# Kernel optimization log

Hardware: AMD Instinct MI355X
Metric: run time of the kernel (lower is better)

Reference implementation:

```python
import jax, jax.numpy as jnp
from jax import lax
import numpy as np

H = 32  # hidden_size


def setup_inputs() -> dict:
    key = jax.random.key(0)
    ks = jax.random.split(key, 12)
    B, T, I = 4096, 1024, 1
    s = lambda fan_in: 1.0 / np.sqrt(fan_in)
    inp = {
        "x": jax.random.normal(ks[0], (B, I, T), dtype=jnp.float32),
        # LSTM params, PyTorch layout: gates stacked as [i, f, g, o]
        "W_ih": jax.random.uniform(ks[1], (4 * H, I), jnp.float32, -s(H), s(H)),
        "W_hh": jax.random.uniform(ks[2], (4 * H, H), jnp.float32, -s(H), s(H)),
        "b_ih": jax.random.uniform(ks[3], (4 * H,), jnp.float32, -s(H), s(H)),
        "b_hh": jax.random.uniform(ks[4], (4 * H,), jnp.float32, -s(H), s(H)),
        # MLP head: 32 -> 16 -> 8 -> 1
        "W1": jax.random.uniform(ks[5], (16, H), jnp.float32, -s(H), s(H)),
        "b1": jax.random.uniform(ks[6], (16,), jnp.float32, -s(H), s(H)),
        "W2": jax.random.uniform(ks[7], (8, 16), jnp.float32, -s(16), s(16)),
        "b2": jax.random.uniform(ks[8], (8,), jnp.float32, -s(16), s(16)),
        "W3": jax.random.uniform(ks[9], (1, 8), jnp.float32, -s(8), s(8)),
        "b3": jax.random.uniform(ks[10], (1,), jnp.float32, -s(8), s(8)),
    }
    return inp


def reference(x, W_ih, W_hh, b_ih, b_hh, W1, b1, W2, b2, W3, b3):
    # x: (B, 1, T) -> (B, T, 1), batch_first LSTM over T
    xs = jnp.transpose(x, (0, 2, 1))
    B, T, _ = xs.shape
    # Precompute input contribution to all gates: (B, T, 4H)
    xW = jnp.einsum('bti,gi->btg', xs, W_ih) + (b_ih + b_hh)

    def step(carry, xw_t):
        h, c = carry
        gates = xw_t + h @ W_hh.T  # (B, 4H)
        i, f, g, o = jnp.split(gates, 4, axis=-1)
        c = jax.nn.sigmoid(f) * c + jax.nn.sigmoid(i) * jnp.tanh(g)
        h = jax.nn.sigmoid(o) * jnp.tanh(c)
        return (h, c), None

    h0 = jnp.zeros((B, H), xs.dtype)
    (h_n, _), _ = lax.scan(step, (h0, h0), jnp.swapaxes(xW, 0, 1))

    # MLP head on final hidden state h_n[-1] (single layer -> h_n itself)
    out = jax.nn.relu(h_n @ W1.T + b1)
    out = jax.nn.relu(out @ W2.T + b2)
    return out @ W3.T + b3  # (B, 1)
```

## Files before the change

### kernel.cpp

```cpp
#include <hip/hip_runtime.h>

#define HSZ 32
#define TT  1024

__device__ __forceinline__ float frcp(float x) { return __builtin_amdgcn_rcpf(x); }
__device__ __forceinline__ float sigm(float z) { return frcp(1.0f + __expf(-z)); }
__device__ __forceinline__ float tanhf_(float z) {
  z = fminf(fmaxf(z, -15.0f), 15.0f);
  float e = __expf(-2.0f * z);
  return (1.0f - e) * frcp(1.0f + e);
}

__global__ __launch_bounds__(256, 2)
void lstm_fused_kernel(const float* __restrict__ x,
                       const float* __restrict__ W_ih,
                       const float* __restrict__ W_hh,
                       const float* __restrict__ b_ih,
                       const float* __restrict__ b_hh,
                       const float* __restrict__ W1, const float* __restrict__ b1,
                       const float* __restrict__ W2, const float* __restrict__ b2,
                       const float* __restrict__ W3, const float* __restrict__ b3,
                       float* __restrict__ out)
{
  __shared__ __align__(16) float hlds[8][HSZ];

  const int tid  = threadIdx.x;
  const int wave = tid >> 6;
  const int lane = tid & 63;
  const int grp  = lane >> 5;
  const int j    = lane & 31;
  const int we   = wave * 2 + grp;
  const int elem = blockIdx.x * 8 + we;

  float w0[HSZ], w1[HSZ], w2[HSZ], w3[HSZ];
  {
    const float4* r0 = reinterpret_cast<const float4*>(W_hh + (0 * 32 + j) * HSZ);
    const float4* r1 = reinterpret_cast<const float4*>(W_hh + (1 * 32 + j) * HSZ);
    const float4* r2 = reinterpret_cast<const float4*>(W_hh + (2 * 32 + j) * HSZ);
    const float4* r3 = reinterpret_cast<const float4*>(W_hh + (3 * 32 + j) * HSZ);
#pragma unroll
    for (int k4 = 0; k4 < 8; ++k4) {
      float4 a = r0[k4]; w0[4*k4+0]=a.x; w0[4*k4+1]=a.y; w0[4*k4+2]=a.z; w0[4*k4+3]=a.w;
      float4 b = r1[k4]; w1[4*k4+0]=b.x; w1[4*k4+1]=b.y; w1[4*k4+2]=b.z; w1[4*k4+3]=b.w;
      float4 c4= r2[k4]; w2[4*k4+0]=c4.x;w2[4*k4+1]=c4.y;w2[4*k4+2]=c4.z;w2[4*k4+3]=c4.w;
      float4 d = r3[k4]; w3[4*k4+0]=d.x; w3[4*k4+1]=d.y; w3[4*k4+2]=d.z; w3[4*k4+3]=d.w;
    }
  }
  const float bi0 = b_ih[0 * 32 + j] + b_hh[0 * 32 + j];
  const float bi1 = b_ih[1 * 32 + j] + b_hh[1 * 32 + j];
  const float bi2 = b_ih[2 * 32 + j] + b_hh[2 * 32 + j];
  const float bi3 = b_ih[3 * 32 + j] + b_hh[3 * 32 + j];
  const float wx0 = W_ih[0 * 32 + j];
  const float wx1 = W_ih[1 * 32 + j];
  const float wx2 = W_ih[2 * 32 + j];
  const float wx3 = W_ih[3 * 32 + j];

  float h[HSZ];
#pragma unroll
  for (int k = 0; k < HSZ; ++k) h[k] = 0.0f;
  float c = 0.0f;

  const float* xrow = x + (size_t)elem * TT;

#pragma unroll 1
  for (int t0 = 0; t0 < TT; t0 += 32) {
    float xc = xrow[t0 + j];
#pragma unroll 1
    for (int s = 0; s < 32; ++s) {
      float xt = __shfl(xc, s, 32);
      float a0 = fmaf(xt, wx0, bi0);
      float a1 = fmaf(xt, wx1, bi1);
      float a2 = fmaf(xt, wx2, bi2);
      float a3 = fmaf(xt, wx3, bi3);
#pragma unroll
      for (int k = 0; k < HSZ; ++k) {
        a0 = fmaf(w0[k], h[k], a0);
        a1 = fmaf(w1[k], h[k], a1);
        a2 = fmaf(w2[k], h[k], a2);
        a3 = fmaf(w3[k], h[k], a3);
      }
      float si = sigm(a0);
      float sf = sigm(a1);
      float tg = tanhf_(a2);
      float so = sigm(a3);
      c = fmaf(sf, c, si * tg);
      float hj = so * tanhf_(c);

      hlds[we][j] = hj;
#pragma unroll
      for (int k4 = 0; k4 < 8; ++k4) {
        float4 v = *reinterpret_cast<const float4*>(&hlds[we][4 * k4]);
        h[4*k4+0] = v.x; h[4*k4+1] = v.y; h[4*k4+2] = v.z; h[4*k4+3] = v.w;
      }
    }
  }

  float a1v[16];
#pragma unroll
  for (int r = 0; r < 16; ++r) {
    float acc = b1[r];
#pragma unroll
    for (int k = 0; k < 32; ++k) acc = fmaf(W1[r * 32 + k], h[k], acc);
    a1v[r] = fmaxf(acc, 0.0f);
  }
  float a2v[8];
#pragma unroll
  for (int r = 0; r < 8; ++r) {
    float acc = b2[r];
#pragma unroll
    for (int k = 0; k < 16; ++k) acc = fmaf(W2[r * 16 + k], a1v[k], acc);
    a2v[r] = fmaxf(acc, 0.0f);
  }
  float o = b3[0];
#pragma unroll
  for (int k = 0; k < 8; ++k) o = fmaf(W3[k], a2v[k], o);

  if (j == 0) out[elem] = o;
}

extern "C" void kernel_launch(void* const* d_in, const int* in_sizes, int n_in,
                              void* d_out, int out_size, void* d_ws, size_t ws_size,
                              hipStream_t stream) {
  const float* x    = (const float*)d_in[0];
  const float* W_ih = (const float*)d_in[1];
  const float* W_hh = (const float*)d_in[2];
  const float* b_ih = (const float*)d_in[3];
  const float* b_hh = (const float*)d_in[4];
  const float* W1   = (const float*)d_in[5];
  const float* b1   = (const float*)d_in[6];
  const float* W2   = (const float*)d_in[7];
  const float* b2   = (const float*)d_in[8];
  const float* W3   = (const float*)d_in[9];
  const float* b3   = (const float*)d_in[10];
  float* out = (float*)d_out;

  const int B = in_sizes[0] / TT;
  dim3 grid(B / 8), block(256);
  hipLaunchKernelGGL(lstm_fused_kernel, grid, block, 0, stream,
                     x, W_ih, W_hh, b_ih, b_hh, W1, b1, W2, b2, W3, b3, out);
}
```

Measured before the change: 597.1 us.

## Process two independent sequences per thread group to interleave recurrences

Each 32-lane group now advances two independent batch elements per time step, reusing the register-resident W_hh across both and giving the scheduler two independent dependency chains to interleave. The grid is halved and launch bounds drop to one block per SIMD pair, so each thread has more registers for the doubled hidden-state arrays. The tanh is also simplified to a 2*sigmoid(2z)-1 form without clamping. The cost is more register pressure and fewer resident waves, which may reduce latency hiding.

Result: slower. 746.2 us (+25.0%).

```diff
diff --git a/kernel.cpp b/kernel.cpp
--- a/kernel.cpp
+++ b/kernel.cpp
@@ -5,13 +5,38 @@
 
 __device__ __forceinline__ float frcp(float x) { return __builtin_amdgcn_rcpf(x); }
 __device__ __forceinline__ float sigm(float z) { return frcp(1.0f + __expf(-z)); }
-__device__ __forceinline__ float tanhf_(float z) {
-  z = fminf(fmaxf(z, -15.0f), 15.0f);
-  float e = __expf(-2.0f * z);
-  return (1.0f - e) * frcp(1.0f + e);
+__device__ __forceinline__ float tanh_(float z) {
+  return fmaf(2.0f, frcp(1.0f + __expf(-2.0f * z)), -1.0f);
 }
 
-__global__ __launch_bounds__(256, 2)
+__device__ __forceinline__ float mlp_tail(const float* hrow,
+                                          const float* __restrict__ W1, const float* __restrict__ b1,
+                                          const float* __restrict__ W2, const float* __restrict__ b2,
+                                          const float* __restrict__ W3, const float* __restrict__ b3)
+{
+  float a1v[16];
+#pragma unroll
+  for (int r = 0; r < 16; ++r) {
+    float acc = b1[r];
+#pragma unroll
+    for (int k = 0; k < 32; ++k) acc = fmaf(W1[r * 32 + k], hrow[k], acc);
+    a1v[r] = fmaxf(acc, 0.0f);
+  }
+  float a2v[8];
+#pragma unroll
+  for (int r = 0; r < 8; ++r) {
+    float acc = b2[r];
+#pragma unroll
+    for (int k = 0; k < 16; ++k) acc = fmaf(W2[r * 16 + k], a1v[k], acc);
+    a2v[r] = fmaxf(acc, 0.0f);
+  }
+  float o = b3[0];
+#pragma unroll
+  for (int k = 0; k < 8; ++k) o = fmaf(W3[k], a2v[k], o);
+  return o;
+}
+
+__global__ __launch_bounds__(256, 1)
 void lstm_fused_kernel(const float* __restrict__ x,
                        const float* __restrict__ W_ih,
                        const float* __restrict__ W_hh,
@@ -22,15 +47,17 @@
                        const float* __restrict__ W3, const float* __restrict__ b3,
                        float* __restrict__ out)
 {
-  __shared__ __align__(16) float hlds[8][HSZ];
+  __shared__ __align__(16) float hlds[16][HSZ];
 
   const int tid  = threadIdx.x;
   const int wave = tid >> 6;
   const int lane = tid & 63;
   const int grp  = lane >> 5;
   const int j    = lane & 31;
-  const int we   = wave * 2 + grp;
-  const int elem = blockIdx.x * 8 + we;
+  const int rowA = wave * 4 + grp;
+  const int rowB = wave * 4 + 2 + grp;
+  const int elemA = blockIdx.x * 16 + rowA;
+  const int elemB = blockIdx.x * 16 + rowB;
 
   float w0[HSZ], w1[HSZ], w2[HSZ], w3[HSZ];
   {
@@ -55,67 +82,78 @@
   const float wx2 = W_ih[2 * 32 + j];
   const float wx3 = W_ih[3 * 32 + j];
 
-  float h[HSZ];
+  float hA[HSZ], hB[HSZ];
 #pragma unroll
-  for (int k = 0; k < HSZ; ++k) h[k] = 0.0f;
-  float c = 0.0f;
+  for (int k = 0; k < HSZ; ++k) { hA[k] = 0.0f; hB[k] = 0.0f; }
+  float cA = 0.0f, cB = 0.0f;
 
-  const float* xrow = x + (size_t)elem * TT;
+  const float* xrowA = x + (size_t)elemA * TT;
+  const float* xrowB = x + (size_t)elemB * TT;
 
 #pragma unroll 1
   for (int t0 = 0; t0 < TT; t0 += 32) {
-    float xc = xrow[t0 + j];
+    float xcA = xrowA[t0 + j];
+    float xcB = xrowB[t0 + j];
 #pragma unroll 1
     for (int s = 0; s < 32; ++s) {
-      float xt = __shfl(xc, s, 32);
-      float a0 = fmaf(xt, wx0, bi0);
-      float a1 = fmaf(xt, wx1, bi1);
-      float a2 = fmaf(xt, wx2, bi2);
-      float a3 = fmaf(xt, wx3, bi3);
+      float xtA = __shfl(xcA, s, 32);
+      float xtB = __shfl(xcB, s, 32);
+
+      {
+        float a0 = bi0, a1 = bi1, a2 = bi2, a3 = bi3;
 #pragma unroll
-      for (int k = 0; k < HSZ; ++k) {
-        a0 = fmaf(w0[k], h[k], a0);
-        a1 = fmaf(w1[k], h[k], a1);
-        a2 = fmaf(w2[k], h[k], a2);
-        a3 = fmaf(w3[k], h[k], a3);
+        for (int k = 0; k < HSZ; ++k) {
+          a0 = fmaf(w0[k], hA[k], a0);
+          a1 = fmaf(w1[k], hA[k], a1);
+          a2 = fmaf(w2[k], hA[k], a2);
+          a3 = fmaf(w3[k], hA[k], a3);
+        }
+        a0 = fmaf(xtA, wx0, a0);
+        a1 = fmaf(xtA, wx1, a1);
+        a2 = fmaf(xtA, wx2, a2);
+        a3 = fmaf(xtA, wx3, a3);
+        float si = sigm(a0), sf = sigm(a1), tg = tanh_(a2), so = sigm(a3);
+        cA = fmaf(sf, cA, si * tg);
+        float hj = so * tanh_(cA);
+        hlds[rowA][j] = hj;
+#pragma unroll
+        for (int k4 = 0; k4 < 8; ++k4) {
+          float4 v = *reinterpret_cast<const float4*>(&hlds[rowA][4 * k4]);
+          hA[4*k4+0] = v.x; hA[4*k4+1] = v.y; hA[4*k4+2] = v.z; hA[4*k4+3] = v.w;
+        }
       }
-      float si = sigm(a0);
-      float sf = sigm(a1);
-      float tg = tanhf_(a2);
-      float so = sigm(a3);
-      c = fmaf(sf, c, si * tg);
-      float hj = so * tanhf_(c);
-
-      hlds[we][j] = hj;
+      {
+        float a0 = bi0, a1 = bi1, a2 = bi2, a3 = bi3;
 #pragma unroll
-      for (int k4 = 0; k4 < 8; ++k4) {
-        float4 v = *reinterpret_cast<const float4*>(&hlds[we][4 * k4]);
-        h[4*k4+0] = v.x; h[4*k4+1] = v.y; h[4*k4+2] = v.z; h[4*k4+3] = v.w;
+        for (int k = 0; k < HSZ; ++k) {
+          a0 = fmaf(w0[k], hB[k], a0);
+          a1 = fmaf(w1[k], hB[k], a1);
+          a2 = fmaf(w2[k], hB[k], a2);
+          a3 = fmaf(w3[k], hB[k], a3);
+        }
+        a0 = fmaf(xtB, wx0, a0);
+        a1 = fmaf(xtB, wx1, a1);
+        a2 = fmaf(xtB, wx2, a2);
+        a3 = fmaf(xtB, wx3, a3);
+        float si = sigm(a0), sf = sigm(a1), tg = tanh_(a2), so = sigm(a3);
+        cB = fmaf(sf, cB, si * tg);
+        float hj = so * tanh_(cB);
+        hlds[rowB][j] = hj;
+#pragma unroll
+        for (int k4 = 0; k4 < 8; ++k4) {
+          float4 v = *reinterpret_cast<const float4*>(&hlds[rowB][4 * k4]);
+          hB[4*k4+0] = v.x; hB[4*k4+1] = v.y; hB[4*k4+2] = v.z; hB[4*k4+3] = v.w;
+        }
       }
     }
   }
 
-  float a1v[16];
-#pragma unroll
-  for (int r = 0; r < 16; ++r) {
-    float acc = b1[r];
-#pragma unroll
-    for (int k = 0; k < 32; ++k) acc = fmaf(W1[r * 32 + k], h[k], acc);
-    a1v[r] = fmaxf(acc, 0.0f);
+  float oA = mlp_tail(&hlds[rowA][0], W1, b1, W2, b2, W3, b3);
+  float oB = mlp_tail(&hlds[rowB][0], W1, b1, W2, b2, W3, b3);
+  if (j == 0) {
+    out[elemA] = oA;
+    out[elemB] = oB;
   }
-  float a2v[8];
-#pragma unroll
-  for (int r = 0; r < 8; ++r) {
-    float acc = b2[r];
-#pragma unroll
-    for (int k = 0; k < 16; ++k) acc = fmaf(W2[r * 16 + k], a1v[k], acc);
-    a2v[r] = fmaxf(acc, 0.0f);
-  }
-  float o = b3[0];
-#pragma unroll
-  for (int k = 0; k < 8; ++k) o = fmaf(W3[k], a2v[k], o);
-
-  if (j == 0) out[elem] = o;
 }
 
 extern "C" void kernel_launch(void* const* d_in, const int* in_sizes, int n_in,
@@ -135,7 +173,7 @@
   float* out = (float*)d_out;
 
   const int B = in_sizes[0] / TT;
-  dim3 grid(B / 8), block(256);
+  dim3 grid(B / 16), block(256);
   hipLaunchKernelGGL(lstm_fused_kernel, grid, block, 0, stream,
                      x, W_ih, W_hh, b_ih, b_hh, W1, b1, W2, b2, W3, b3, out);
 }
```
